# Performance work log

Measured on AMD Instinct MI355X. Metric: run time of the kernel, lower is better.

The kernel has to match this reference:

```python
import jax, jax.numpy as jnp
import numpy as np

D = 128
RANK = 16
N_USER, N_PROD, N_CAT, N_BRAND = 100000, 100000, 1000, 2000
E_BEH, E_STR = 100000, 50000
NODE_TYPES = ['user', 'product', 'category', 'brand']
N_NODES = {'user': N_USER, 'product': N_PROD, 'category': N_CAT, 'brand': N_BRAND}
PHI = {'user': 0, 'product': 1, 'category': 2, 'brand': 3}
# (src_type, edge_name, dst_type, rel_idx, beta or None for structural)
EDGE_META = [
    ('user', 'view', 'product', 0, 0),
    ('user', 'cart', 'product', 1, 1),
    ('user', 'purchase', 'product', 2, 2),
    ('product', 'rev_view', 'user', 3, 0),
    ('product', 'rev_cart', 'user', 4, 1),
    ('product', 'rev_purchase', 'user', 5, 2),
    ('product', 'belongs_to', 'category', 6, None),
    ('category', 'contains', 'product', 7, None),
    ('product', 'producedBy', 'brand', 8, None),
    ('brand', 'brands', 'product', 9, None),
]


def setup_inputs() -> dict:
    key = jax.random.key(0)
    ks = iter(jax.random.split(key, 64))
    inp = {}
    for t in NODE_TYPES:
        inp['x_' + t] = jax.random.normal(next(ks), (N_NODES[t], D), jnp.float32)
    for (st, name, dt, ridx, beta) in EDGE_META:
        E = E_BEH if beta is not None else E_STR
        src = jax.random.randint(next(ks), (E,), 0, N_NODES[st], jnp.int32)
        dst = jax.random.randint(next(ks), (E,), 0, N_NODES[dt], jnp.int32)
        inp['ei_' + name] = jnp.stack([src, dst])
        if beta is None:
            inp['attr_' + name] = jax.random.randint(next(ks), (E,), 0, 3, jnp.int32)
    s = 0.05
    inp['W_base'] = jax.random.normal(next(ks), (D, D), jnp.float32) * s
    inp['A'] = jax.random.normal(next(ks), (4, D, RANK), jnp.float32) * s
    inp['B'] = jax.random.normal(next(ks), (4, D, RANK), jnp.float32) * s
    inp['rel_W'] = jax.random.normal(next(ks), (10, D), jnp.float32) * s
    inp['beh_W'] = jax.random.normal(next(ks), (4, D), jnp.float32) * s
    inp['a_att'] = jax.random.normal(next(ks), (4 * D,), jnp.float32) * s
    inp['ln_gamma'] = jnp.ones((D,), jnp.float32)
    inp['ln_beta'] = jnp.zeros((D,), jnp.float32)
    return inp


def _forward(x, eis, attrs, W_base, A, B, rel_W, beh_W, a_att, ln_gamma, ln_beta):
    a0, a1, a2, a3 = a_att[:D], a_att[D:2 * D], a_att[2 * D:3 * D], a_att[3 * D:]
    agg = {t: jnp.zeros((N_NODES[t], D), x['user'].dtype) for t in NODE_TYPES}
    for (src_t, name, dst_t, ridx, beta) in EDGE_META:
        ei = eis[name]
        src, dst = ei[0], ei[1]
        hs = x[src_t][src]            # [E, D] gather
        hd = x[dst_t][dst]            # [E, D] gather
        phi = PHI[src_t]
        if beta is not None:
            # uniform behavior beta: W = W_base + A_phi @ B_beta^T
            W = W_base + A[phi] @ B[beta].T
            msg = hs @ W.T
            hproj = hd @ W.T
            b_term = (beh_W[beta] * a3).sum()
        else:
            # per-edge behavior origin from edge_attr (clamped to {0,1,2})
            origin = jnp.clip(attrs[name].reshape(-1), 0, 2)
            mids = jnp.einsum('ei,bir->ebr', hs, B[:3])            # [E, 3, rank]
            mid = jnp.take_along_axis(mids, origin[:, None, None], axis=1)[:, 0, :]
            msg = hs @ W_base.T + mid @ A[phi].T
            hproj = hd @ W_base.T
            b_term = (beh_W[origin] * a3).sum(-1)                  # [E]
        r_scalar = (rel_W[ridx] * a2).sum()
        e = (msg * a0).sum(-1) + (hproj * a1).sum(-1) + r_scalar + b_term
        # destination-grouped softmax over edges
        n_dst = N_NODES[dst_t]
        m = jax.ops.segment_max(e, dst, num_segments=n_dst)
        ex = jnp.exp(e - m[dst])
        ssum = jax.ops.segment_sum(ex, dst, num_segments=n_dst)
        alpha = ex / (ssum[dst] + 1e-16)
        agg[dst_t] = agg[dst_t] + jax.ops.segment_sum(alpha[:, None] * msg, dst, num_segments=n_dst)
    outs = []
    for t in NODE_TYPES:
        h = agg[t]
        mu = h.mean(-1, keepdims=True)
        var = ((h - mu) ** 2).mean(-1, keepdims=True)
        hn = (h - mu) / jnp.sqrt(var + 1e-5) * ln_gamma + ln_beta
        outs.append(jax.nn.elu(hn + x[t]))   # residual: in_dim == out_dim
    return jnp.concatenate(outs, axis=0)     # [N_user+N_prod+N_cat+N_brand, D]


def reference(x_user, x_product, x_category, x_brand,
              ei_view, ei_cart, ei_purchase, ei_rev_view, ei_rev_cart, ei_rev_purchase,
              ei_belongs_to, ei_contains, ei_producedBy, ei_brands,
              attr_belongs_to, attr_contains, attr_producedBy, attr_brands,
              W_base, A, B, rel_W, beh_W, a_att, ln_gamma, ln_beta):
    x = {'user': x_user, 'product': x_product, 'category': x_category, 'brand': x_brand}
    eis = {'view': ei_view, 'cart': ei_cart, 'purchase': ei_purchase,
           'rev_view': ei_rev_view, 'rev_cart': ei_rev_cart, 'rev_purchase': ei_rev_purchase,
           'belongs_to': ei_belongs_to, 'contains': ei_contains,
           'producedBy': ei_producedBy, 'brands': ei_brands}
    attrs = {'belongs_to': attr_belongs_to, 'contains': attr_contains,
             'producedBy': attr_producedBy, 'brands': attr_brands}
    return _forward(x, eis, attrs, W_base, A, B, rel_W, beh_W, a_att, ln_gamma, ln_beta)
```

## Files before the change

### kernel.cpp

```cpp
#include <hip/hip_runtime.h>
#include <hip/hip_bf16.h>
#include <math.h>

#define D 128

#define NU 100000
#define NP 100000
#define NC 1000
#define NB 2000
#define NTOT 203000
#define EB 100000
#define ES 50000
#define ETOT 800000
#define NSEG 803000
#define NBLK 785

#define OFF_L    0
#define OFF_W0   6448000
#define OFF_BS   6451840
#define OFF_WT   7251856
#define OFF_AT   7268240
#define OFF_INT  7276432

__constant__ int c_srcT[10]   = {0,0,0,1,1,1,1,2,1,3};
__constant__ int c_phi [10]   = {0,0,0,1,1,1,1,2,1,3};
__constant__ int c_beta[10]   = {0,1,2,0,1,2,-1,-1,-1,-1};
__constant__ int c_E   [10]   = {EB,EB,EB,EB,EB,EB,ES,ES,ES,ES};
__constant__ int c_moff[10]   = {0,100000,200000,300000,400000,500000,600000,601000,701000,703000};

__constant__ int g_nGrp[4]    = {1,3,1,1};
__constant__ int g_Loff[4][3] = {{1600000,0,0},{0,3216000,4848000},{3200000,0,0},{4816000,0,0}};
__constant__ int g_ai[4][3]   = {{1,0,0},{0,2,3},{1,0,0},{1,0,0}};

#define K4_BU 782
#define K4_BP 1564
#define K4_BC 1572
#define K4_BT 1588

struct Ptrs {
    const float* x[4];
    const int*   ei[10];
    const int*   attr[4];
};

__device__ __forceinline__ void decode_et(int eflat, int& et, int& le) {
    if (eflat < 600000) { et = eflat / 100000; le = eflat - et * 100000; }
    else { int r = eflat - 600000; int q = r / 50000; et = 6 + q; le = r - q * 50000; }
}

__device__ __forceinline__ float qsum(float v) {
    v += __shfl_xor(v, 1, 64);
    v += __shfl_xor(v, 2, 64);
    v += __shfl_xor(v, 4, 64);
    v += __shfl_xor(v, 8, 64);
    return v;
}

__global__ void k0_tables(const float* __restrict__ Wb, const float* __restrict__ A,
                          const float* __restrict__ B, const float* __restrict__ behW,
                          const float* __restrict__ a_att,
                          float* __restrict__ w0, float* __restrict__ bs_out)
{
    __shared__ float a0[128];
    __shared__ float c0[128];
    __shared__ float g0[4][16];
    int t = threadIdx.x;
    if (t < 128) a0[t] = a_att[t];
    __syncthreads();
    if (t < 128) {
        float s0=0.f;
        for (int j=0;j<128;j++) s0 += Wb[j*128+t]*a0[j];
        c0[t]=s0;
    } else if (t < 192) {
        int q=t-128, p=q>>4, r=q&15;
        float s0=0.f;
        for (int i=0;i<128;i++) s0 += A[p*2048+i*16+r]*a0[i];
        g0[p][r]=s0;
    } else if (t < 196) {
        int b=t-192; float s=0.f;
        for (int i=0;i<128;i++) s += behW[b*128+i]*a_att[384+i];
        bs_out[b]=s;
    }
    __syncthreads();
    if (t < 128) {
        for (int et=0; et<10; ++et) {
            int phi=c_phi[et], beta=c_beta[et];
            if (beta >= 0) {
                float s0=c0[t];
                for (int r=0;r<16;r++) s0 += B[beta*2048+t*16+r]*g0[phi][r];
                w0[et*384+t]=s0; w0[et*384+128+t]=s0; w0[et*384+256+t]=s0;
            } else {
                for (int o=0;o<3;o++){
                    float s0=c0[t];
                    for (int r=0;r<16;r++) s0 += B[o*2048+t*16+r]*g0[phi][r];
                    w0[et*384+o*128+t]=s0;
                }
            }
        }
    }
}

__global__ __launch_bounds__(256) void ktrans(const float* __restrict__ Wb,
        const float* __restrict__ A, float* __restrict__ WbT, float* __restrict__ AT)
{
    int idx = blockIdx.x*256 + threadIdx.x;
    if (idx < 16384) { int i = idx>>7, j = idx&127; WbT[i*128+j] = Wb[j*128+i]; }
    int idx2 = idx - 16384;
    if (idx2 >= 0 && idx2 < 8192) {
        int p = idx2>>11, rem = idx2&2047, r = rem>>7, j = rem&127;
        AT[idx2] = A[p*2048 + j*16 + r];
    }
}

__global__ __launch_bounds__(256) void khist(Ptrs P, int* __restrict__ counts)
{
    int eflat = blockIdx.x*256 + threadIdx.x;
    if (eflat >= ETOT) return;
    int et, le; decode_et(eflat, et, le);
    int dst = P.ei[et][c_E[et] + le];
    atomicAdd(&counts[c_moff[et] + dst], 1);
}

__global__ __launch_bounds__(256) void kscan1(const int* __restrict__ cnt,
                                              int* __restrict__ st, int* __restrict__ bsums)
{
    __shared__ int lds[256];
    int t = threadIdx.x, b = blockIdx.x;
    int base = b*1024 + t*4;
    int v0 = (base   < NSEG) ? cnt[base]   : 0;
    int v1 = (base+1 < NSEG) ? cnt[base+1] : 0;
    int v2 = (base+2 < NSEG) ? cnt[base+2] : 0;
    int v3 = (base+3 < NSEG) ? cnt[base+3] : 0;
    int s = v0+v1+v2+v3;
    lds[t] = s; __syncthreads();
    for (int off=1; off<256; off<<=1){
        int xv = (t>=off) ? lds[t-off] : 0;
        __syncthreads();
        lds[t] += xv;
        __syncthreads();
    }
    int incl = lds[t];
    int p = incl - s;
    if (t==255) bsums[b] = incl;
    if (base   < NSEG) st[base]   = p; p += v0;
    if (base+1 < NSEG) st[base+1] = p; p += v1;
    if (base+2 < NSEG) st[base+2] = p; p += v2;
    if (base+3 < NSEG) st[base+3] = p;
}

__global__ __launch_bounds__(256) void kscan2(int* __restrict__ bsums)
{
    __shared__ int lds[256];
    int t = threadIdx.x;
    int base = t*4;
    int v0 = (base   < NBLK) ? bsums[base]   : 0;
    int v1 = (base+1 < NBLK) ? bsums[base+1] : 0;
    int v2 = (base+2 < NBLK) ? bsums[base+2] : 0;
    int v3 = (base+3 < NBLK) ? bsums[base+3] : 0;
    int s = v0+v1+v2+v3;
    lds[t] = s; __syncthreads();
    for (int off=1; off<256; off<<=1){
        int xv = (t>=off) ? lds[t-off] : 0;
        __syncthreads();
        lds[t] += xv;
        __syncthreads();
    }
    int p = lds[t] - s;
    if (base   < NBLK) bsums[base]   = p; p += v0;
    if (base+1 < NBLK) bsums[base+1] = p; p += v1;
    if (base+2 < NBLK) bsums[base+2] = p; p += v2;
    if (base+3 < NBLK) bsums[base+3] = p;
}

__global__ __launch_bounds__(256) void kscan3(int* __restrict__ st, const int* __restrict__ bsums)
{
    int t = threadIdx.x, b = blockIdx.x;
    int add = bsums[b];
    int base = b*1024 + t*4;
    #pragma unroll
    for (int j=0;j<4;j++)
        if (base+j < NSEG) st[base+j] += add;
}

__global__ __launch_bounds__(256) void kscatter(Ptrs P, int* __restrict__ st, int* __restrict__ srco)
{
    int eflat = blockIdx.x*256 + threadIdx.x;
    if (eflat >= ETOT) return;
    int et, le; decode_et(eflat, et, le);
    const int* ei = P.ei[et];
    int E = c_E[et];
    int src = ei[le], dst = ei[E+le];
    int o;
    if (et >= 6) { int a = P.attr[et-6][le]; o = min(max(a,0),2); }
    else o = c_beta[et];
    int pos = atomicAdd(&st[c_moff[et] + dst], 1);
    srco[pos] = src | (o<<17) | (et<<19);
}

__global__ __launch_bounds__(256) void kagg_beh(Ptrs P,
        const int* __restrict__ starts, const int* __restrict__ counts,
        const int* __restrict__ srco,
        const float* __restrict__ w0, const float* __restrict__ Bm,
        float* __restrict__ Sout, float* __restrict__ Lb, int nWaves)
{
    int lane = threadIdx.x & 63;
    int wv = (blockIdx.x * 256 + threadIdx.x) >> 6;
    int grp = lane >> 4, ln = lane & 15;

    for (int nid = wv; nid < NU + NP; nid += nWaves) {
        int T = (nid < NU) ? 0 : 1;
        int n0 = (T == 0) ? nid : nid - NU;
        int etBase = (T == 0) ? 3 : 0;
        const float* xs = P.x[1 - T];

        int sgA = c_moff[etBase] + n0;
        int cnt0 = counts[sgA],        cnt1 = counts[sgA+100000], cnt2 = counts[sgA+200000];
        int sa0  = starts[sgA]-cnt0,   sa1  = starts[sgA+100000]-cnt1, sa2 = starts[sgA+200000]-cnt2;
        int sv1 = (grp < cnt1) ? srco[sa1+grp] : 0;
        int sv2 = (grp < cnt2) ? srco[sa2+grp] : 0;
        float4 pA = make_float4(0.f,0.f,0.f,0.f), pB = pA;
        if (grp < cnt0) {
            int sv0 = srco[sa0+grp];
            const float* q = xs + (size_t)(sv0 & 0x1FFFF)*D + ln*8;
            pA = *(const float4*)q; pB = *(const float4*)(q+4);
        }

        float Stot[8] = {0,0,0,0,0,0,0,0};
        float Lq0=0.f, Lq1=0.f, Lq2=0.f, Lq3=0.f;

        for (int s=0; s<3; ++s) {
            int cnt = (s==0)?cnt0:((s==1)?cnt1:cnt2);
            int st0 = (s==0)?sa0:((s==1)?sa1:sa2);
            float4 cA = pA, cB = pB;
            pA = make_float4(0.f,0.f,0.f,0.f); pB = pA;
            if (s == 0) {
                if (grp < cnt1) {
                    const float* q = xs + (size_t)(sv1 & 0x1FFFF)*D + ln*8;
                    pA = *(const float4*)q; pB = *(const float4*)(q+4);
                }
            } else if (s == 1) {
                if (grp < cnt2) {
                    const float* q = xs + (size_t)(sv2 & 0x1FFFF)*D + ln*8;
                    pA = *(const float4*)q; pB = *(const float4*)(q+4);
                }
            }
            if (cnt == 0) continue;
            int et = etBase + s;
            const float* wq = w0 + et*384 + ln*8;
            float4 wA = *(const float4*)wq, wB = *(const float4*)(wq+4);

            float ssum = 0.f;
            float SA[8] = {0,0,0,0,0,0,0,0};

            for (int k0=0; k0<cnt; k0+=4) {
                bool act = (k0+grp) < cnt;
                if (k0 > 0) {
                    cA = make_float4(0.f,0.f,0.f,0.f); cB = cA;
                    if (act) {
                        int sv = srco[st0+k0+grp];
                        const float* q = xs + (size_t)(sv & 0x1FFFF)*D + ln*8;
                        cA = *(const float4*)q; cB = *(const float4*)(q+4);
                    }
                }
                float d = cA.x*wA.x + cA.y*wA.y + cA.z*wA.z + cA.w*wA.w
                        + cB.x*wB.x + cB.y*wB.y + cB.z*wB.z + cB.w*wB.w;
                d = qsum(d);
                float wg = act ? __expf(d) : 0.f;
                ssum += wg;
                SA[0]+=wg*cA.x; SA[1]+=wg*cA.y; SA[2]+=wg*cA.z; SA[3]+=wg*cA.w;
                SA[4]+=wg*cB.x; SA[5]+=wg*cB.y; SA[6]+=wg*cB.z; SA[7]+=wg*cB.w;
            }
            ssum += __shfl_xor(ssum, 16, 64);
            ssum += __shfl_xor(ssum, 32, 64);
            float inv = 1.f/(ssum + 1e-16f);
            #pragma unroll
            for (int j=0;j<8;j++){ SA[j] += __shfl_xor(SA[j],16,64); SA[j] += __shfl_xor(SA[j],32,64); }
            #pragma unroll
            for (int j=0;j<8;j++) Stot[j] += SA[j]*inv;

            const float* Bp = Bm + s*2048 + grp*4;
            float p0=0.f,p1=0.f,p2=0.f,p3=0.f;
            #pragma unroll
            for (int j=0;j<8;j++){
                float4 b4 = *(const float4*)(Bp + (ln*8+j)*16);
                float v = SA[j];
                p0+=v*b4.x; p1+=v*b4.y; p2+=v*b4.z; p3+=v*b4.w;
            }
            Lq0 += qsum(p0)*inv; Lq1 += qsum(p1)*inv;
            Lq2 += qsum(p2)*inv; Lq3 += qsum(p3)*inv;
        }

        if (grp == 0) {
            float* Srow = Sout + (size_t)nid*D + ln*8;
            *(float4*)Srow     = make_float4(Stot[0],Stot[1],Stot[2],Stot[3]);
            *(float4*)(Srow+4) = make_float4(Stot[4],Stot[5],Stot[6],Stot[7]);
        }
        if (ln < 4) {
            float v = (ln==0)?Lq0:((ln==1)?Lq1:((ln==2)?Lq2:Lq3));
            int loff = (T==0) ? 1600000 : 0;
            Lb[loff + (size_t)n0*16 + grp*4 + ln] = v;
        }
    }
}

__global__ __launch_bounds__(256) void kagg_str(Ptrs P,
        const int* __restrict__ starts, const int* __restrict__ counts,
        const int* __restrict__ srco,
        const float* __restrict__ w0, const float* __restrict__ bs,
        const float* __restrict__ Bm,
        float* __restrict__ Sout, float* __restrict__ Lb, int nWaves)
{
    int lane = threadIdx.x & 63;
    int wv = (blockIdx.x * 256 + threadIdx.x) >> 6;
    int grp = lane >> 4, ln = lane & 15;
    float bs0 = bs[0], bs1 = bs[1], bs2 = bs[2];

    for (int id = wv; id < NP + NC + NB; id += nWaves) {
        int T, n0, nseg;
        if (id < NP) { T=1; n0=id; nseg=2; }
        else if (id < NP+NC) { T=2; n0=id-NP; nseg=1; }
        else { T=3; n0=id-(NP+NC); nseg=1; }
        int outRow = (T==1) ? (100000+n0) : ((T==2) ? (200000+n0) : (201000+n0));

        float Stot[8] = {0,0,0,0,0,0,0,0};

        for (int s=0; s<nseg; ++s) {
            int et = (T==1) ? (s==0 ? 7 : 9) : ((T==2) ? 6 : 8);
            int seg = c_moff[et] + n0;
            int cnt = counts[seg];
            int st0 = starts[seg] - cnt;
            const float* xs = P.x[c_srcT[et]];
            const float* wbase = w0 + et*384;

            float ssum = 0.f;
            float SA[8]={0,0,0,0,0,0,0,0}, SB[8]={0,0,0,0,0,0,0,0}, SC[8]={0,0,0,0,0,0,0,0};
            int fa=0, fb=0, fc=0;

            for (int k0=0; k0<cnt; k0+=4) {
                bool act = (k0+grp) < cnt;
                int sv = act ? srco[st0+k0+grp] : 0;
                int o = (sv>>17)&3;
                float4 hA = make_float4(0.f,0.f,0.f,0.f), hB = hA;
                if (act) {
                    const float* q = xs + (size_t)(sv & 0x1FFFF)*D + ln*8;
                    hA = *(const float4*)q; hB = *(const float4*)(q+4);
                }
                const float* wq = wbase + o*128 + ln*8;
                float4 wA = *(const float4*)wq, wB = *(const float4*)(wq+4);
                float d = hA.x*wA.x + hA.y*wA.y + hA.z*wA.z + hA.w*wA.w
                        + hB.x*wB.x + hB.y*wB.y + hB.z*wB.z + hB.w*wB.w;
                d = qsum(d);
                float wg = act ? __expf(d + ((o==0)?bs0:((o==1)?bs1:bs2))) : 0.f;
                ssum += wg;
                fa |= (int)(act && (o==0)); fb |= (int)(act && (o==1)); fc |= (int)(act && (o==2));
                float wg0=(o==0)?wg:0.f, wg1=(o==1)?wg:0.f, wg2=(o==2)?wg:0.f;
                #pragma unroll
                for (int j=0;j<8;j++){
                    float hj = (j==0)?hA.x:(j==1)?hA.y:(j==2)?hA.z:(j==3)?hA.w:
                               (j==4)?hB.x:(j==5)?hB.y:(j==6)?hB.z:hB.w;
                    SA[j] += wg0*hj; SB[j] += wg1*hj; SC[j] += wg2*hj;
                }
            }

            ssum += __shfl_xor(ssum, 16, 64);
            ssum += __shfl_xor(ssum, 32, 64);
            float inv = 1.f/(ssum + 1e-16f);

            int anyA = __any(fa), anyB = __any(fb), anyC = __any(fc);
            if (anyA) {
                #pragma unroll
                for (int j=0;j<8;j++){ SA[j] += __shfl_xor(SA[j],16,64); SA[j] += __shfl_xor(SA[j],32,64); }
            }
            if (anyB) {
                #pragma unroll
                for (int j=0;j<8;j++){ SB[j] += __shfl_xor(SB[j],16,64); SB[j] += __shfl_xor(SB[j],32,64); }
            }
            if (anyC) {
                #pragma unroll
                for (int j=0;j<8;j++){ SC[j] += __shfl_xor(SC[j],16,64); SC[j] += __shfl_xor(SC[j],32,64); }
            }
            #pragma unroll
            for (int j=0;j<8;j++) Stot[j] += (SA[j]+SB[j]+SC[j])*inv;

            float p0=0.f,p1=0.f,p2=0.f,p3=0.f;
            if (anyA) {
                const float* Bp = Bm + grp*4;
                #pragma unroll
                for (int j=0;j<8;j++){
                    float4 b4 = *(const float4*)(Bp + (ln*8+j)*16);
                    float v = SA[j];
                    p0+=v*b4.x; p1+=v*b4.y; p2+=v*b4.z; p3+=v*b4.w;
                }
            }
            if (anyB) {
                const float* Bp = Bm + 2048 + grp*4;
                #pragma unroll
                for (int j=0;j<8;j++){
                    float4 b4 = *(const float4*)(Bp + (ln*8+j)*16);
                    float v = SB[j];
                    p0+=v*b4.x; p1+=v*b4.y; p2+=v*b4.z; p3+=v*b4.w;
                }
            }
            if (anyC) {
                const float* Bp = Bm + 4096 + grp*4;
                #pragma unroll
                for (int j=0;j<8;j++){
                    float4 b4 = *(const float4*)(Bp + (ln*8+j)*16);
                    float v = SC[j];
                    p0+=v*b4.x; p1+=v*b4.y; p2+=v*b4.z; p3+=v*b4.w;
                }
            }
            p0 = qsum(p0)*inv; p1 = qsum(p1)*inv; p2 = qsum(p2)*inv; p3 = qsum(p3)*inv;

            int loff = (T==1) ? (s==0 ? 3216000 : 4848000) : ((T==2) ? 3200000 : 4816000);
            if (ln < 4) {
                float v = (ln==0)?p0:((ln==1)?p1:((ln==2)?p2:p3));
                Lb[loff + (size_t)n0*16 + grp*4 + ln] = v;
            }
        }

        if (grp == 0) {
            float* Srow = Sout + (size_t)outRow*D + ln*8;
            if (T == 1) {
                float4 a = *(const float4*)Srow, b = *(const float4*)(Srow+4);
                *(float4*)Srow     = make_float4(a.x+Stot[0],a.y+Stot[1],a.z+Stot[2],a.w+Stot[3]);
                *(float4*)(Srow+4) = make_float4(b.x+Stot[4],b.y+Stot[5],b.z+Stot[6],b.w+Stot[7]);
            } else {
                *(float4*)Srow     = make_float4(Stot[0],Stot[1],Stot[2],Stot[3]);
                *(float4*)(Srow+4) = make_float4(Stot[4],Stot[5],Stot[6],Stot[7]);
            }
        }
    }
}

__global__ __launch_bounds__(512, 1) void k4_final(Ptrs P,
        const float* __restrict__ WbT, const float* __restrict__ AT,
        const float* __restrict__ Lb,
        const float* __restrict__ gamma, const float* __restrict__ lbeta,
        float* __restrict__ out)
{
    __shared__ float st[128*132];
    __shared__ float wt[128*128];
    __shared__ float lt[128*52];
    int t = threadIdx.x;
    int b = blockIdx.x;
    int T, lb;
    if (b < K4_BU)      { T=0; lb=b; }
    else if (b < K4_BP) { T=1; lb=b-K4_BU; }
    else if (b < K4_BC) { T=2; lb=b-K4_BP; }
    else                { T=3; lb=b-K4_BC; }
    int r0 = lb*128;
    int rowStart = (T==0)?0:((T==1)?100000:((T==2)?200000:201000));
    int nRows    = (T==0)?NU:((T==1)?NP:((T==2)?NC:NB));
    const float* x = P.x[T];
    int nPairs = g_nGrp[T];

    for (int idx=t; idx<4096; idx+=512)
        *(float4*)&wt[idx*4] = *(const float4*)&WbT[idx*4];
    for (int idx=t; idx<4096; idx+=512){
        int r = idx>>5, i4 = idx&31;
        int lr = r0 + r;
        float4 v = (lr < nRows) ? *(const float4*)&out[(size_t)(rowStart+lr)*D + i4*4]
                                : make_float4(0.f,0.f,0.f,0.f);
        *(float4*)&st[r*132 + i4*4] = v;
    }
    for (int pi=0; pi<nPairs; ++pi){
        int lo = g_Loff[T][pi];
        int r = t>>2, q = t&3;
        int lr = r0 + r;
        float4 v = (lr < nRows) ? *(const float4*)&Lb[lo + (size_t)lr*16 + q*4]
                                : make_float4(0.f,0.f,0.f,0.f);
        *(float4*)&lt[r*52 + pi*16 + q*4] = v;
    }
    __syncthreads();

    int cg = t & 15, rg = t >> 4;
    float acc[4][8];
    #pragma unroll
    for (int a=0;a<4;a++)
        #pragma unroll
        for (int c=0;c<8;c++) acc[a][c]=0.f;

    for (int i4=0; i4<32; ++i4){
        float4 sv0 = *(const float4*)&st[(rg*4+0)*132 + i4*4];
        float4 sv1 = *(const float4*)&st[(rg*4+1)*132 + i4*4];
        float4 sv2 = *(const float4*)&st[(rg*4+2)*132 + i4*4];
        float4 sv3 = *(const float4*)&st[(rg*4+3)*132 + i4*4];
        #pragma unroll
        for (int q=0;q<4;q++){
            float4 wA = *(const float4*)&wt[(i4*4+q)*128 + cg*4];
            float4 wB = *(const float4*)&wt[(i4*4+q)*128 + 64 + cg*4];
            float sq[4];
            sq[0] = (q==0)?sv0.x:(q==1)?sv0.y:(q==2)?sv0.z:sv0.w;
            sq[1] = (q==0)?sv1.x:(q==1)?sv1.y:(q==2)?sv1.z:sv1.w;
            sq[2] = (q==0)?sv2.x:(q==1)?sv2.y:(q==2)?sv2.z:sv2.w;
            sq[3] = (q==0)?sv3.x:(q==1)?sv3.y:(q==2)?sv3.z:sv3.w;
            #pragma unroll
            for (int rr=0;rr<4;rr++){
                acc[rr][0] += sq[rr]*wA.x;
                acc[rr][1] += sq[rr]*wA.y;
                acc[rr][2] += sq[rr]*wA.z;
                acc[rr][3] += sq[rr]*wA.w;
                acc[rr][4] += sq[rr]*wB.x;
                acc[rr][5] += sq[rr]*wB.y;
                acc[rr][6] += sq[rr]*wB.z;
                acc[rr][7] += sq[rr]*wB.w;
            }
        }
    }

    for (int pi=0; pi<nPairs; ++pi){
        int ai = g_ai[T][pi];
        const float* Ap = AT + ai*2048;
        #pragma unroll 4
        for (int r=0;r<16;++r){
            float4 aA = *(const float4*)&Ap[r*128 + cg*4];
            float4 aB = *(const float4*)&Ap[r*128 + 64 + cg*4];
            float lv[4];
            #pragma unroll
            for (int rr=0;rr<4;rr++) lv[rr] = lt[(rg*4+rr)*52 + pi*16 + r];
            #pragma unroll
            for (int rr=0;rr<4;rr++){
                acc[rr][0] += lv[rr]*aA.x;
                acc[rr][1] += lv[rr]*aA.y;
                acc[rr][2] += lv[rr]*aA.z;
                acc[rr][3] += lv[rr]*aA.w;
                acc[rr][4] += lv[rr]*aB.x;
                acc[rr][5] += lv[rr]*aB.y;
                acc[rr][6] += lv[rr]*aB.z;
                acc[rr][7] += lv[rr]*aB.w;
            }
        }
    }

    int jA = cg*4, jB = 64 + cg*4;
    float4 gA = *(const float4*)&gamma[jA], gB = *(const float4*)&gamma[jB];
    float4 bA = *(const float4*)&lbeta[jA], bB = *(const float4*)&lbeta[jB];
    float gv[8] = {gA.x,gA.y,gA.z,gA.w,gB.x,gB.y,gB.z,gB.w};
    float bv[8] = {bA.x,bA.y,bA.z,bA.w,bB.x,bB.y,bB.z,bB.w};

    #pragma unroll
    for (int rr=0;rr<4;rr++){
        int lr = r0 + rg*4 + rr;
        float lsum=0.f, lsq=0.f;
        #pragma unroll
        for (int c=0;c<8;c++){ lsum += acc[rr][c]; lsq += acc[rr][c]*acc[rr][c]; }
        #pragma unroll
        for (int mm=1; mm<16; mm<<=1){ lsum += __shfl_xor(lsum,mm,64); lsq += __shfl_xor(lsq,mm,64); }
        if (lr >= nRows) continue;
        float mu = lsum*(1.f/128.f);
        float var = lsq*(1.f/128.f) - mu*mu;
        float rstd = rsqrtf(var + 1e-5f);
        const float* xr = x + (size_t)lr*D;
        float4 xA = *(const float4*)(xr+jA), xB = *(const float4*)(xr+jB);
        float xv[8] = {xA.x,xA.y,xA.z,xA.w,xB.x,xB.y,xB.z,xB.w};
        float ov[8];
        #pragma unroll
        for (int c=0;c<8;c++){
            float hn = (acc[rr][c]-mu)*rstd*gv[c] + bv[c];
            float z = hn + xv[c];
            ov[c] = z > 0.f ? z : expm1f(z);
        }
        float* orow = out + (size_t)(rowStart+lr)*D;
        *(float4*)(orow+jA) = make_float4(ov[0],ov[1],ov[2],ov[3]);
        *(float4*)(orow+jB) = make_float4(ov[4],ov[5],ov[6],ov[7]);
    }
}

extern "C" void kernel_launch(void* const* d_in, const int* in_sizes, int n_in,
                              void* d_out, int out_size, void* d_ws, size_t ws_size,
                              hipStream_t stream)
{
    (void)in_sizes; (void)n_in; (void)out_size; (void)ws_size;
    Ptrs P;
    P.x[0] = (const float*)d_in[0];
    P.x[1] = (const float*)d_in[1];
    P.x[2] = (const float*)d_in[2];
    P.x[3] = (const float*)d_in[3];
    P.ei[0] = (const int*)d_in[4];
    P.ei[1] = (const int*)d_in[5];
    P.ei[2] = (const int*)d_in[6];
    P.ei[3] = (const int*)d_in[7];
    P.ei[4] = (const int*)d_in[8];
    P.ei[5] = (const int*)d_in[9];
    P.ei[6] = (const int*)d_in[10];
    P.attr[0] = (const int*)d_in[11];
    P.ei[7] = (const int*)d_in[12];
    P.attr[1] = (const int*)d_in[13];
    P.ei[8] = (const int*)d_in[14];
    P.attr[2] = (const int*)d_in[15];
    P.ei[9] = (const int*)d_in[16];
    P.attr[3] = (const int*)d_in[17];
    const float* Wb    = (const float*)d_in[18];
    const float* A     = (const float*)d_in[19];
    const float* B     = (const float*)d_in[20];
    const float* behW  = (const float*)d_in[22];
    const float* a_att = (const float*)d_in[23];
    const float* gamma = (const float*)d_in[24];
    const float* lbeta = (const float*)d_in[25];
    float* wsf = (float*)d_ws;
    float* out = (float*)d_out;

    int* ip     = (int*)(wsf + OFF_INT);
    int* counts = ip;
    int* starts = ip + 803000;
    int* srco   = ip + 1606000;
    int* bsums  = (int*)wsf;

    hipMemsetAsync(counts, 0, (size_t)NSEG*sizeof(int), stream);

    k0_tables<<<1, 256, 0, stream>>>(Wb, A, B, behW, a_att, wsf+OFF_W0, wsf+OFF_BS);
    ktrans<<<96, 256, 0, stream>>>(Wb, A, wsf+OFF_WT, wsf+OFF_AT);
    khist<<<3125, 256, 0, stream>>>(P, counts);
    kscan1<<<NBLK, 256, 0, stream>>>(counts, starts, bsums);
    kscan2<<<1, 256, 0, stream>>>(bsums);
    kscan3<<<NBLK, 256, 0, stream>>>(starts, bsums);
    kscatter<<<3125, 256, 0, stream>>>(P, starts, srco);

    kagg_beh<<<2048, 256, 0, stream>>>(P, starts, counts, srco,
                                       wsf+OFF_W0, B, out, wsf+OFF_L, 2048*4);
    kagg_str<<<1024, 256, 0, stream>>>(P, starts, counts, srco,
                                       wsf+OFF_W0, wsf+OFF_BS, B, out, wsf+OFF_L, 1024*4);

    k4_final<<<K4_BT, 512, 0, stream>>>(P, wsf+OFF_WT, wsf+OFF_AT, wsf+OFF_L,
                                        gamma, lbeta, out);
}
```

Baseline: 893.3 us.

## Fuse behavioral and structural aggregation kernels into one launch with separate product buffer

Merges the two aggregation kernels into one grid-stride kernel over all destination nodes. Product structural sums now go to a separate zeroed buffer S2 that the final kernel adds in, removing the read-modify-write ordering dependency on the output. Product nodes with no structural edges are skipped, relying on memsets of the L buffer and S2. The price is two extra memsets (about 51MB for S2) and an extra S2 read in the final kernel.

```diff
diff --git a/kernel.cpp b/kernel.cpp
--- a/kernel.cpp
+++ b/kernel.cpp
@@ -14,6 +14,7 @@
 #define ETOT 800000
 #define NSEG 803000
 #define NBLK 785
+#define NID_ALL 303000
 
 #define OFF_L    0
 #define OFF_W0   6448000
@@ -21,6 +22,7 @@
 #define OFF_WT   7251856
 #define OFF_AT   7268240
 #define OFF_INT  7276432
+#define OFF_S2   9682432
 
 __constant__ int c_srcT[10]   = {0,0,0,1,1,1,1,2,1,3};
 __constant__ int c_phi [10]   = {0,0,0,1,1,1,1,2,1,3};
@@ -197,245 +199,256 @@
     srco[pos] = src | (o<<17) | (et<<19);
 }
 
-__global__ __launch_bounds__(256) void kagg_beh(Ptrs P,
-        const int* __restrict__ starts, const int* __restrict__ counts,
-        const int* __restrict__ srco,
-        const float* __restrict__ w0, const float* __restrict__ Bm,
-        float* __restrict__ Sout, float* __restrict__ Lb, int nWaves)
-{
-    int lane = threadIdx.x & 63;
-    int wv = (blockIdx.x * 256 + threadIdx.x) >> 6;
-    int grp = lane >> 4, ln = lane & 15;
-
-    for (int nid = wv; nid < NU + NP; nid += nWaves) {
-        int T = (nid < NU) ? 0 : 1;
-        int n0 = (T == 0) ? nid : nid - NU;
-        int etBase = (T == 0) ? 3 : 0;
-        const float* xs = P.x[1 - T];
-
-        int sgA = c_moff[etBase] + n0;
-        int cnt0 = counts[sgA],        cnt1 = counts[sgA+100000], cnt2 = counts[sgA+200000];
-        int sa0  = starts[sgA]-cnt0,   sa1  = starts[sgA+100000]-cnt1, sa2 = starts[sgA+200000]-cnt2;
-        int sv1 = (grp < cnt1) ? srco[sa1+grp] : 0;
-        int sv2 = (grp < cnt2) ? srco[sa2+grp] : 0;
-        float4 pA = make_float4(0.f,0.f,0.f,0.f), pB = pA;
-        if (grp < cnt0) {
-            int sv0 = srco[sa0+grp];
-            const float* q = xs + (size_t)(sv0 & 0x1FFFF)*D + ln*8;
-            pA = *(const float4*)q; pB = *(const float4*)(q+4);
-        }
-
-        float Stot[8] = {0,0,0,0,0,0,0,0};
-        float Lq0=0.f, Lq1=0.f, Lq2=0.f, Lq3=0.f;
-
-        for (int s=0; s<3; ++s) {
-            int cnt = (s==0)?cnt0:((s==1)?cnt1:cnt2);
-            int st0 = (s==0)?sa0:((s==1)?sa1:sa2);
-            float4 cA = pA, cB = pB;
-            pA = make_float4(0.f,0.f,0.f,0.f); pB = pA;
-            if (s == 0) {
-                if (grp < cnt1) {
-                    const float* q = xs + (size_t)(sv1 & 0x1FFFF)*D + ln*8;
-                    pA = *(const float4*)q; pB = *(const float4*)(q+4);
-                }
-            } else if (s == 1) {
-                if (grp < cnt2) {
-                    const float* q = xs + (size_t)(sv2 & 0x1FFFF)*D + ln*8;
-                    pA = *(const float4*)q; pB = *(const float4*)(q+4);
-                }
-            }
-            if (cnt == 0) continue;
-            int et = etBase + s;
-            const float* wq = w0 + et*384 + ln*8;
-            float4 wA = *(const float4*)wq, wB = *(const float4*)(wq+4);
-
-            float ssum = 0.f;
-            float SA[8] = {0,0,0,0,0,0,0,0};
-
-            for (int k0=0; k0<cnt; k0+=4) {
-                bool act = (k0+grp) < cnt;
-                if (k0 > 0) {
-                    cA = make_float4(0.f,0.f,0.f,0.f); cB = cA;
-                    if (act) {
-                        int sv = srco[st0+k0+grp];
-                        const float* q = xs + (size_t)(sv & 0x1FFFF)*D + ln*8;
-                        cA = *(const float4*)q; cB = *(const float4*)(q+4);
-                    }
-                }
-                float d = cA.x*wA.x + cA.y*wA.y + cA.z*wA.z + cA.w*wA.w
-                        + cB.x*wB.x + cB.y*wB.y + cB.z*wB.z + cB.w*wB.w;
-                d = qsum(d);
-                float wg = act ? __expf(d) : 0.f;
-                ssum += wg;
-                SA[0]+=wg*cA.x; SA[1]+=wg*cA.y; SA[2]+=wg*cA.z; SA[3]+=wg*cA.w;
-                SA[4]+=wg*cB.x; SA[5]+=wg*cB.y; SA[6]+=wg*cB.z; SA[7]+=wg*cB.w;
-            }
-            ssum += __shfl_xor(ssum, 16, 64);
-            ssum += __shfl_xor(ssum, 32, 64);
-            float inv = 1.f/(ssum + 1e-16f);
-            #pragma unroll
-            for (int j=0;j<8;j++){ SA[j] += __shfl_xor(SA[j],16,64); SA[j] += __shfl_xor(SA[j],32,64); }
-            #pragma unroll
-            for (int j=0;j<8;j++) Stot[j] += SA[j]*inv;
-
-            const float* Bp = Bm + s*2048 + grp*4;
-            float p0=0.f,p1=0.f,p2=0.f,p3=0.f;
-            #pragma unroll
-            for (int j=0;j<8;j++){
-                float4 b4 = *(const float4*)(Bp + (ln*8+j)*16);
-                float v = SA[j];
-                p0+=v*b4.x; p1+=v*b4.y; p2+=v*b4.z; p3+=v*b4.w;
-            }
-            Lq0 += qsum(p0)*inv; Lq1 += qsum(p1)*inv;
-            Lq2 += qsum(p2)*inv; Lq3 += qsum(p3)*inv;
-        }
-
-        if (grp == 0) {
-            float* Srow = Sout + (size_t)nid*D + ln*8;
-            *(float4*)Srow     = make_float4(Stot[0],Stot[1],Stot[2],Stot[3]);
-            *(float4*)(Srow+4) = make_float4(Stot[4],Stot[5],Stot[6],Stot[7]);
-        }
-        if (ln < 4) {
-            float v = (ln==0)?Lq0:((ln==1)?Lq1:((ln==2)?Lq2:Lq3));
-            int loff = (T==0) ? 1600000 : 0;
-            Lb[loff + (size_t)n0*16 + grp*4 + ln] = v;
-        }
-    }
-}
-
-__global__ __launch_bounds__(256) void kagg_str(Ptrs P,
+__device__ __forceinline__ void str_seg(int cnt, int st0, int hv,
+        const int* __restrict__ srco, const float* __restrict__ xs,
+        const float* __restrict__ wbase, float bs0, float bs1, float bs2,
+        const float* __restrict__ Bm, int grp, int ln,
+        float Stot[8], float* __restrict__ Lrow)
+{
+    if (cnt == 0) return;
+    float ssum = 0.f;
+    float SA[8]={0,0,0,0,0,0,0,0}, SB[8]={0,0,0,0,0,0,0,0}, SC[8]={0,0,0,0,0,0,0,0};
+    int fa=0, fb=0, fc=0;
+
+    for (int k0=0; k0<cnt; k0+=4) {
+        bool act = (k0+grp) < cnt;
+        int sv = (k0 == 0) ? hv : (act ? srco[st0+k0+grp] : 0);
+        int o = (sv>>17)&3;
+        float4 hA = make_float4(0.f,0.f,0.f,0.f), hB = hA;
+        if (act) {
+            const float* q = xs + (size_t)(sv & 0x1FFFF)*D + ln*8;
+            hA = *(const float4*)q; hB = *(const float4*)(q+4);
+        }
+        const float* wq = wbase + o*128 + ln*8;
+        float4 wA = *(const float4*)wq, wB = *(const float4*)(wq+4);
+        float d = hA.x*wA.x + hA.y*wA.y + hA.z*wA.z + hA.w*wA.w
+                + hB.x*wB.x + hB.y*wB.y + hB.z*wB.z + hB.w*wB.w;
+        d = qsum(d);
+        float wg = act ? __expf(d + ((o==0)?bs0:((o==1)?bs1:bs2))) : 0.f;
+        ssum += wg;
+        fa |= (int)(act && (o==0)); fb |= (int)(act && (o==1)); fc |= (int)(act && (o==2));
+        float wg0=(o==0)?wg:0.f, wg1=(o==1)?wg:0.f, wg2=(o==2)?wg:0.f;
+        #pragma unroll
+        for (int j=0;j<8;j++){
+            float hj = (j==0)?hA.x:(j==1)?hA.y:(j==2)?hA.z:(j==3)?hA.w:
+                       (j==4)?hB.x:(j==5)?hB.y:(j==6)?hB.z:hB.w;
+            SA[j] += wg0*hj; SB[j] += wg1*hj; SC[j] += wg2*hj;
+        }
+    }
+
+    ssum += __shfl_xor(ssum, 16, 64);
+    ssum += __shfl_xor(ssum, 32, 64);
+    float inv = 1.f/(ssum + 1e-16f);
+
+    int anyA = __any(fa), anyB = __any(fb), anyC = __any(fc);
+    if (anyA) {
+        #pragma unroll
+        for (int j=0;j<8;j++){ SA[j] += __shfl_xor(SA[j],16,64); SA[j] += __shfl_xor(SA[j],32,64); }
+    }
+    if (anyB) {
+        #pragma unroll
+        for (int j=0;j<8;j++){ SB[j] += __shfl_xor(SB[j],16,64); SB[j] += __shfl_xor(SB[j],32,64); }
+    }
+    if (anyC) {
+        #pragma unroll
+        for (int j=0;j<8;j++){ SC[j] += __shfl_xor(SC[j],16,64); SC[j] += __shfl_xor(SC[j],32,64); }
+    }
+    #pragma unroll
+    for (int j=0;j<8;j++) Stot[j] += (SA[j]+SB[j]+SC[j])*inv;
+
+    float p0=0.f,p1=0.f,p2=0.f,p3=0.f;
+    if (anyA) {
+        const float* Bp = Bm + grp*4;
+        #pragma unroll
+        for (int j=0;j<8;j++){
+            float4 b4 = *(const float4*)(Bp + (ln*8+j)*16);
+            float v = SA[j];
+            p0+=v*b4.x; p1+=v*b4.y; p2+=v*b4.z; p3+=v*b4.w;
+        }
+    }
+    if (anyB) {
+        const float* Bp = Bm + 2048 + grp*4;
+        #pragma unroll
+        for (int j=0;j<8;j++){
+            float4 b4 = *(const float4*)(Bp + (ln*8+j)*16);
+            float v = SB[j];
+            p0+=v*b4.x; p1+=v*b4.y; p2+=v*b4.z; p3+=v*b4.w;
+        }
+    }
+    if (anyC) {
+        const float* Bp = Bm + 4096 + grp*4;
+        #pragma unroll
+        for (int j=0;j<8;j++){
+            float4 b4 = *(const float4*)(Bp + (ln*8+j)*16);
+            float v = SC[j];
+            p0+=v*b4.x; p1+=v*b4.y; p2+=v*b4.z; p3+=v*b4.w;
+        }
+    }
+    p0 = qsum(p0)*inv; p1 = qsum(p1)*inv; p2 = qsum(p2)*inv; p3 = qsum(p3)*inv;
+    if (ln < 4) {
+        float v = (ln==0)?p0:((ln==1)?p1:((ln==2)?p2:p3));
+        Lrow[grp*4 + ln] = v;
+    }
+}
+
+__global__ __launch_bounds__(256) void kagg_all(Ptrs P,
         const int* __restrict__ starts, const int* __restrict__ counts,
         const int* __restrict__ srco,
         const float* __restrict__ w0, const float* __restrict__ bs,
         const float* __restrict__ Bm,
-        float* __restrict__ Sout, float* __restrict__ Lb, int nWaves)
+        float* __restrict__ Sout, float* __restrict__ S2,
+        float* __restrict__ Lb, int nWaves)
 {
     int lane = threadIdx.x & 63;
     int wv = (blockIdx.x * 256 + threadIdx.x) >> 6;
     int grp = lane >> 4, ln = lane & 15;
     float bs0 = bs[0], bs1 = bs[1], bs2 = bs[2];
 
-    for (int id = wv; id < NP + NC + NB; id += nWaves) {
-        int T, n0, nseg;
-        if (id < NP) { T=1; n0=id; nseg=2; }
-        else if (id < NP+NC) { T=2; n0=id-NP; nseg=1; }
-        else { T=3; n0=id-(NP+NC); nseg=1; }
-        int outRow = (T==1) ? (100000+n0) : ((T==2) ? (200000+n0) : (201000+n0));
-
-        float Stot[8] = {0,0,0,0,0,0,0,0};
-
-        for (int s=0; s<nseg; ++s) {
-            int et = (T==1) ? (s==0 ? 7 : 9) : ((T==2) ? 6 : 8);
-            int seg = c_moff[et] + n0;
-            int cnt = counts[seg];
-            int st0 = starts[seg] - cnt;
-            const float* xs = P.x[c_srcT[et]];
-            const float* wbase = w0 + et*384;
-
-            float ssum = 0.f;
-            float SA[8]={0,0,0,0,0,0,0,0}, SB[8]={0,0,0,0,0,0,0,0}, SC[8]={0,0,0,0,0,0,0,0};
-            int fa=0, fb=0, fc=0;
-
-            for (int k0=0; k0<cnt; k0+=4) {
-                bool act = (k0+grp) < cnt;
-                int sv = act ? srco[st0+k0+grp] : 0;
-                int o = (sv>>17)&3;
-                float4 hA = make_float4(0.f,0.f,0.f,0.f), hB = hA;
-                if (act) {
-                    const float* q = xs + (size_t)(sv & 0x1FFFF)*D + ln*8;
-                    hA = *(const float4*)q; hB = *(const float4*)(q+4);
+    for (int id = wv; id < NID_ALL; id += nWaves) {
+        if (id < 200000) {
+            int T = (id < NU) ? 0 : 1;
+            int n0 = (T == 0) ? id : id - NU;
+            int etBase = (T == 0) ? 3 : 0;
+            const float* xs = P.x[1 - T];
+
+            int sgA = c_moff[etBase] + n0;
+            int cnt0 = counts[sgA],        cnt1 = counts[sgA+100000], cnt2 = counts[sgA+200000];
+            int sa0  = starts[sgA]-cnt0,   sa1  = starts[sgA+100000]-cnt1, sa2 = starts[sgA+200000]-cnt2;
+            int sv1 = (grp < cnt1) ? srco[sa1+grp] : 0;
+            int sv2 = (grp < cnt2) ? srco[sa2+grp] : 0;
+            float4 pA = make_float4(0.f,0.f,0.f,0.f), pB = pA;
+            if (grp < cnt0) {
+                int sv0 = srco[sa0+grp];
+                const float* q = xs + (size_t)(sv0 & 0x1FFFF)*D + ln*8;
+                pA = *(const float4*)q; pB = *(const float4*)(q+4);
+            }
+
+            float Stot[8] = {0,0,0,0,0,0,0,0};
+            float Lq0=0.f, Lq1=0.f, Lq2=0.f, Lq3=0.f;
+
+            for (int s=0; s<3; ++s) {
+                int cnt = (s==0)?cnt0:((s==1)?cnt1:cnt2);
+                int st0 = (s==0)?sa0:((s==1)?sa1:sa2);
+                float4 cA = pA, cB = pB;
+                pA = make_float4(0.f,0.f,0.f,0.f); pB = pA;
+                if (s == 0) {
+                    if (grp < cnt1) {
+                        const float* q = xs + (size_t)(sv1 & 0x1FFFF)*D + ln*8;
+                        pA = *(const float4*)q; pB = *(const float4*)(q+4);
+                    }
+                } else if (s == 1) {
+                    if (grp < cnt2) {
+                        const float* q = xs + (size_t)(sv2 & 0x1FFFF)*D + ln*8;
+                        pA = *(const float4*)q; pB = *(const float4*)(q+4);
+                    }
                 }
-                const float* wq = wbase + o*128 + ln*8;
+                if (cnt == 0) continue;
+                int et = etBase + s;
+                const float* wq = w0 + et*384 + ln*8;
                 float4 wA = *(const float4*)wq, wB = *(const float4*)(wq+4);
-                float d = hA.x*wA.x + hA.y*wA.y + hA.z*wA.z + hA.w*wA.w
-                        + hB.x*wB.x + hB.y*wB.y + hB.z*wB.z + hB.w*wB.w;
-                d = qsum(d);
-                float wg = act ? __expf(d + ((o==0)?bs0:((o==1)?bs1:bs2))) : 0.f;
-                ssum += wg;
-                fa |= (int)(act && (o==0)); fb |= (int)(act && (o==1)); fc |= (int)(act && (o==2));
-                float wg0=(o==0)?wg:0.f, wg1=(o==1)?wg:0.f, wg2=(o==2)?wg:0.f;
-                #pragma unroll
-                for (int j=0;j<8;j++){
-                    float hj = (j==0)?hA.x:(j==1)?hA.y:(j==2)?hA.z:(j==3)?hA.w:
-                               (j==4)?hB.x:(j==5)?hB.y:(j==6)?hB.z:hB.w;
-                    SA[j] += wg0*hj; SB[j] += wg1*hj; SC[j] += wg2*hj;
+
+                float ssum = 0.f;
+                float SA[8] = {0,0,0,0,0,0,0,0};
+
+                for (int k0=0; k0<cnt; k0+=4) {
+                    bool act = (k0+grp) < cnt;
+                    if (k0 > 0) {
+                        cA = make_float4(0.f,0.f,0.f,0.f); cB = cA;
+                        if (act) {
+                            int sv = srco[st0+k0+grp];
+                            const float* q = xs + (size_t)(sv & 0x1FFFF)*D + ln*8;
+                            cA = *(const float4*)q; cB = *(const float4*)(q+4);
+                        }
+                    }
+                    float d = cA.x*wA.x + cA.y*wA.y + cA.z*wA.z + cA.w*wA.w
+                            + cB.x*wB.x + cB.y*wB.y + cB.z*wB.z + cB.w*wB.w;
+                    d = qsum(d);
+                    float wg = act ? __expf(d) : 0.f;
+                    ssum += wg;
+                    SA[0]+=wg*cA.x; SA[1]+=wg*cA.y; SA[2]+=wg*cA.z; SA[3]+=wg*cA.w;
+                    SA[4]+=wg*cB.x; SA[5]+=wg*cB.y; SA[6]+=wg*cB.z; SA[7]+=wg*cB.w;
                 }
-            }
-
-            ssum += __shfl_xor(ssum, 16, 64);
-            ssum += __shfl_xor(ssum, 32, 64);
-            float inv = 1.f/(ssum + 1e-16f);
-
-            int anyA = __any(fa), anyB = __any(fb), anyC = __any(fc);
-            if (anyA) {
+                ssum += __shfl_xor(ssum, 16, 64);
+                ssum += __shfl_xor(ssum, 32, 64);
+                float inv = 1.f/(ssum + 1e-16f);
                 #pragma unroll
                 for (int j=0;j<8;j++){ SA[j] += __shfl_xor(SA[j],16,64); SA[j] += __shfl_xor(SA[j],32,64); }
-            }
-            if (anyB) {
                 #pragma unroll
-                for (int j=0;j<8;j++){ SB[j] += __shfl_xor(SB[j],16,64); SB[j] += __shfl_xor(SB[j],32,64); }
-            }
-            if (anyC) {
-                #pragma unroll
-                for (int j=0;j<8;j++){ SC[j] += __shfl_xor(SC[j],16,64); SC[j] += __shfl_xor(SC[j],32,64); }
-            }
-            #pragma unroll
-            for (int j=0;j<8;j++) Stot[j] += (SA[j]+SB[j]+SC[j])*inv;
-
-            float p0=0.f,p1=0.f,p2=0.f,p3=0.f;
-            if (anyA) {
-                const float* Bp = Bm + grp*4;
+                for (int j=0;j<8;j++) Stot[j] += SA[j]*inv;
+
+                const float* Bp = Bm + s*2048 + grp*4;
+                float p0=0.f,p1=0.f,p2=0.f,p3=0.f;
                 #pragma unroll
                 for (int j=0;j<8;j++){
                     float4 b4 = *(const float4*)(Bp + (ln*8+j)*16);
                     float v = SA[j];
                     p0+=v*b4.x; p1+=v*b4.y; p2+=v*b4.z; p3+=v*b4.w;
                 }
-            }
-            if (anyB) {
-                const float* Bp = Bm + 2048 + grp*4;
-                #pragma unroll
-                for (int j=0;j<8;j++){
-                    float4 b4 = *(const float4*)(Bp + (ln*8+j)*16);
-                    float v = SB[j];
-                    p0+=v*b4.x; p1+=v*b4.y; p2+=v*b4.z; p3+=v*b4.w;
-                }
-            }
-            if (anyC) {
-                const float* Bp = Bm + 4096 + grp*4;
-                #pragma unroll
-                for (int j=0;j<8;j++){
-                    float4 b4 = *(const float4*)(Bp + (ln*8+j)*16);
-                    float v = SC[j];
-                    p0+=v*b4.x; p1+=v*b4.y; p2+=v*b4.z; p3+=v*b4.w;
-                }
-            }
-            p0 = qsum(p0)*inv; p1 = qsum(p1)*inv; p2 = qsum(p2)*inv; p3 = qsum(p3)*inv;
-
-            int loff = (T==1) ? (s==0 ? 3216000 : 4848000) : ((T==2) ? 3200000 : 4816000);
-            if (ln < 4) {
-                float v = (ln==0)?p0:((ln==1)?p1:((ln==2)?p2:p3));
-                Lb[loff + (size_t)n0*16 + grp*4 + ln] = v;
-            }
-        }
-
-        if (grp == 0) {
-            float* Srow = Sout + (size_t)outRow*D + ln*8;
-            if (T == 1) {
-                float4 a = *(const float4*)Srow, b = *(const float4*)(Srow+4);
-                *(float4*)Srow     = make_float4(a.x+Stot[0],a.y+Stot[1],a.z+Stot[2],a.w+Stot[3]);
-                *(float4*)(Srow+4) = make_float4(b.x+Stot[4],b.y+Stot[5],b.z+Stot[6],b.w+Stot[7]);
-            } else {
+                Lq0 += qsum(p0)*inv; Lq1 += qsum(p1)*inv;
+                Lq2 += qsum(p2)*inv; Lq3 += qsum(p3)*inv;
+            }
+
+            if (grp == 0) {
+                float* Srow = Sout + (size_t)id*D + ln*8;
                 *(float4*)Srow     = make_float4(Stot[0],Stot[1],Stot[2],Stot[3]);
                 *(float4*)(Srow+4) = make_float4(Stot[4],Stot[5],Stot[6],Stot[7]);
             }
+            if (ln < 4) {
+                float v = (ln==0)?Lq0:((ln==1)?Lq1:((ln==2)?Lq2:Lq3));
+                int loff = (T==0) ? 1600000 : 0;
+                Lb[loff + (size_t)n0*16 + grp*4 + ln] = v;
+            }
+        } else if (id < 300000) {
+            int n0 = id - 200000;
+            int seg7 = 601000 + n0, seg9 = 703000 + n0;
+            int cnt7 = counts[seg7], cnt9 = counts[seg9];
+            if ((cnt7 | cnt9) == 0) continue;
+            int st7 = starts[seg7] - cnt7, st9 = starts[seg9] - cnt9;
+            int hv7 = (grp < cnt7) ? srco[st7+grp] : 0;
+            int hv9 = (grp < cnt9) ? srco[st9+grp] : 0;
+
+            float Stot[8] = {0,0,0,0,0,0,0,0};
+            str_seg(cnt7, st7, hv7, srco, P.x[2], w0 + 7*384,
+                    bs0, bs1, bs2, Bm, grp, ln, Stot,
+                    Lb + 3216000 + (size_t)n0*16);
+            str_seg(cnt9, st9, hv9, srco, P.x[3], w0 + 9*384,
+                    bs0, bs1, bs2, Bm, grp, ln, Stot,
+                    Lb + 4848000 + (size_t)n0*16);
+
+            if (grp == 0) {
+                float* Srow = S2 + (size_t)n0*D + ln*8;
+                *(float4*)Srow     = make_float4(Stot[0],Stot[1],Stot[2],Stot[3]);
+                *(float4*)(Srow+4) = make_float4(Stot[4],Stot[5],Stot[6],Stot[7]);
+            }
+        } else {
+            int T = (id < 301000) ? 2 : 3;
+            int n0 = (T==2) ? (id-300000) : (id-301000);
+            int et = (T==2) ? 6 : 8;
+            int outRow = (T==2) ? (200000+n0) : (201000+n0);
+            int seg = c_moff[et] + n0;
+            int cnt = counts[seg];
+            int st0 = starts[seg] - cnt;
+            int hv  = (grp < cnt) ? srco[st0+grp] : 0;
+
+            float Stot[8] = {0,0,0,0,0,0,0,0};
+            int loff = (T==2) ? 3200000 : 4816000;
+            str_seg(cnt, st0, hv, srco, P.x[1], w0 + et*384,
+                    bs0, bs1, bs2, Bm, grp, ln, Stot,
+                    Lb + loff + (size_t)n0*16);
+            if (cnt == 0 && ln < 4) Lb[loff + (size_t)n0*16 + grp*4 + ln] = 0.f;
+
+            if (grp == 0) {
+                float* Srow = Sout + (size_t)outRow*D + ln*8;
+                *(float4*)Srow     = make_float4(Stot[0],Stot[1],Stot[2],Stot[3]);
+                *(float4*)(Srow+4) = make_float4(Stot[4],Stot[5],Stot[6],Stot[7]);
+            }
         }
     }
 }
 
 __global__ __launch_bounds__(512, 1) void k4_final(Ptrs P,
         const float* __restrict__ WbT, const float* __restrict__ AT,
-        const float* __restrict__ Lb,
+        const float* __restrict__ Lb, const float* __restrict__ S2,
         const float* __restrict__ gamma, const float* __restrict__ lbeta,
         float* __restrict__ out)
 {
@@ -460,8 +473,14 @@
     for (int idx=t; idx<4096; idx+=512){
         int r = idx>>5, i4 = idx&31;
         int lr = r0 + r;
-        float4 v = (lr < nRows) ? *(const float4*)&out[(size_t)(rowStart+lr)*D + i4*4]
-                                : make_float4(0.f,0.f,0.f,0.f);
+        float4 v = make_float4(0.f,0.f,0.f,0.f);
+        if (lr < nRows) {
+            v = *(const float4*)&out[(size_t)(rowStart+lr)*D + i4*4];
+            if (T == 1) {
+                float4 w2 = *(const float4*)&S2[(size_t)lr*D + i4*4];
+                v.x += w2.x; v.y += w2.y; v.z += w2.z; v.w += w2.w;
+            }
+        }
         *(float4*)&st[r*132 + i4*4] = v;
     }
     for (int pi=0; pi<nPairs; ++pi){
@@ -606,8 +625,11 @@
     int* starts = ip + 803000;
     int* srco   = ip + 1606000;
     int* bsums  = (int*)wsf;
+    float* S2   = wsf + OFF_S2;
 
     hipMemsetAsync(counts, 0, (size_t)NSEG*sizeof(int), stream);
+    hipMemsetAsync(wsf + 3216000, 0, (size_t)(6448000-3216000)*sizeof(float), stream);
+    hipMemsetAsync(S2, 0, (size_t)12800000*sizeof(float), stream);
 
     k0_tables<<<1, 256, 0, stream>>>(Wb, A, B, behW, a_att, wsf+OFF_W0, wsf+OFF_BS);
     ktrans<<<96, 256, 0, stream>>>(Wb, A, wsf+OFF_WT, wsf+OFF_AT);
@@ -617,11 +639,10 @@
     kscan3<<<NBLK, 256, 0, stream>>>(starts, bsums);
     kscatter<<<3125, 256, 0, stream>>>(P, starts, srco);
 
-    kagg_beh<<<2048, 256, 0, stream>>>(P, starts, counts, srco,
-                                       wsf+OFF_W0, B, out, wsf+OFF_L, 2048*4);
-    kagg_str<<<1024, 256, 0, stream>>>(P, starts, counts, srco,
-                                       wsf+OFF_W0, wsf+OFF_BS, B, out, wsf+OFF_L, 1024*4);
-
-    k4_final<<<K4_BT, 512, 0, stream>>>(P, wsf+OFF_WT, wsf+OFF_AT, wsf+OFF_L,
+    kagg_all<<<4096, 256, 0, stream>>>(P, starts, counts, srco,
+                                       wsf+OFF_W0, wsf+OFF_BS, B,
+                                       out, S2, wsf+OFF_L, 4096*4);
+
+    k4_final<<<K4_BT, 512, 0, stream>>>(P, wsf+OFF_WT, wsf+OFF_AT, wsf+OFF_L, S2,
                                         gamma, lbeta, out);
 }
```

Measured after the change: 887.5 us. Within noise of the previous version (-0.6%).
